# Kernel tuning notes

Measured on AMD Instinct MI355X. Metric: run time of the kernel, lower is better.

The kernel has to match this reference:

```python
import jax, jax.numpy as jnp
import numpy as np

N_ATOMS = 100000   # real atoms (index 0 is padding row -> total rows N_ATOMS+1)
N_BONDS = 200000   # real directed bonds (index 0 is padding row)
MAX_NB = 6
HIDDEN = 300
ATOM_FDIM = 133
BOND_FDIM = 147
DEPTH = 3
N_MOLS = 5000
ATOMS_PER_MOL = N_ATOMS // N_MOLS


def setup_inputs() -> dict:
    key = jax.random.key(0)
    ks = jax.random.split(key, 8)
    f_atoms = jax.random.normal(ks[0], (N_ATOMS + 1, ATOM_FDIM), dtype=jnp.float32)
    f_atoms = f_atoms.at[0].set(0.0)  # chemprop zero-padding row
    f_bonds = jax.random.normal(ks[1], (N_BONDS + 1, BOND_FDIM), dtype=jnp.float32)
    f_bonds = f_bonds.at[0].set(0.0)
    # weights (Linear stored as [in, out]); bias=False for W_i/W_h, W_o has bias
    W_i = jax.random.normal(ks[2], (BOND_FDIM, HIDDEN), dtype=jnp.float32) * 0.05
    W_h = jax.random.normal(ks[3], (HIDDEN, HIDDEN), dtype=jnp.float32) * 0.05
    W_o = jax.random.normal(ks[4], (ATOM_FDIM + HIDDEN, HIDDEN), dtype=jnp.float32) * 0.05
    b_o = jnp.zeros((HIDDEN,), dtype=jnp.float32)
    # a2b: incoming bond ids per atom, padded with 0 (padding row of message is 0)
    a2b = jax.random.randint(ks[5], (N_ATOMS + 1, MAX_NB), 0, N_BONDS + 1, dtype=jnp.int32)
    a2b = a2b.at[0].set(0)
    # b2a: source atom of each bond
    b2a = jax.random.randint(ks[6], (N_BONDS + 1,), 1, N_ATOMS + 1, dtype=jnp.int32)
    b2a = b2a.at[0].set(0)
    # b2revb: reverse-bond pairing; bonds (2k+1, 2k+2) are partners, 0 -> 0
    idx = jnp.arange(N_BONDS + 1, dtype=jnp.int32)
    b2revb = jnp.where(idx == 0, 0, ((idx - 1) ^ 1) + 1).astype(jnp.int32)
    # molecule segment id for each real atom (replaces a_scope loop)
    mol_ids = (jnp.arange(N_ATOMS, dtype=jnp.int32) // ATOMS_PER_MOL).astype(jnp.int32)
    return {"f_atoms": f_atoms, "f_bonds": f_bonds, "W_i": W_i, "W_h": W_h,
            "W_o": W_o, "b_o": b_o, "a2b": a2b, "b2a": b2a, "b2revb": b2revb,
            "mol_ids": mol_ids}


def reference(f_atoms, f_bonds, W_i, W_h, W_o, b_o, a2b, b2a, b2revb, mol_ids):
    # input = act(W_i(f_bonds))  (ReLU, bias=False)
    inp = jax.nn.relu(f_bonds @ W_i)                    # [B+1, H]
    message = inp
    for _ in range(DEPTH - 1):
        nei = message[a2b]                              # [A+1, MAX_NB, H] gather
        a_message = nei.sum(axis=1)                     # [A+1, H]
        message = a_message[b2a] - message[b2revb]      # [B+1, H]
        message = jax.nn.relu(inp + message @ W_h)      # skip-connection + act
    # final atom readout
    a_message = message[a2b].sum(axis=1)                # [A+1, H]
    a_input = jnp.concatenate([f_atoms, a_message], axis=1)
    atom_hiddens = jax.nn.relu(a_input @ W_o + b_o)     # [A+1, H]
    # per-molecule mean pooling over real atoms (rows 1:)
    real = atom_hiddens[1:]                             # [A, H]
    sums = jax.ops.segment_sum(real, mol_ids, num_segments=N_MOLS)
    counts = jax.ops.segment_sum(jnp.ones((N_ATOMS,), dtype=real.dtype), mol_ids,
                                 num_segments=N_MOLS)
    mol_vecs = sums / jnp.maximum(counts, 1.0)[:, None]  # [N_MOLS, H]
    return mol_vecs
```

## Files before the change

### kernel.cpp

```cpp
#include <hip/hip_runtime.h>
#include <hip/hip_bf16.h>

#define N_ATOMS   100000
#define N_BONDS   200000
#define MAX_NB    6
#define HIDDEN    300
#define ATOM_FDIM 133
#define BOND_FDIM 147
#define N_MOLS    5000
#define APM       20

#define MB_ROWS (N_BONDS + 1)
#define MA_ROWS (N_ATOMS + 1)

#define CHUNKS_B 1280
#define EPS      308
#define ROWP     65

typedef unsigned short bf16_t;
typedef __attribute__((ext_vector_type(8))) __bf16 bf16x8;
typedef __attribute__((ext_vector_type(4))) float  float4v;
typedef __attribute__((ext_vector_type(2))) unsigned int uint2v;

__device__ __forceinline__ float bf2f(unsigned short u) {
    union { unsigned int i; float f; } x; x.i = ((unsigned int)u) << 16; return x.f;
}
__device__ __forceinline__ unsigned short f2bf(float f) {
    union { float f; unsigned int i; } x; x.f = f;
    unsigned int r = x.i + 0x7FFFu + ((x.i >> 16) & 1u);
    return (unsigned short)(r >> 16);
}
__device__ __forceinline__ float lo_f(unsigned int u) {
    union { unsigned int i; float f; } x; x.i = u << 16; return x.f;
}
__device__ __forceinline__ float hi_f(unsigned int u) {
    union { unsigned int i; float f; } x; x.i = u & 0xffff0000u; return x.f;
}

__device__ __forceinline__ void gload8(uint2v& d, const void* a) {
    asm volatile("global_load_dwordx2 %0, %1, off"
                 : "=v"(d) : "v"(a) : "memory");
}
#define VM_DRAIN() do {                                      \
    asm volatile("s_waitcnt vmcnt(0)" ::: "memory");         \
    __builtin_amdgcn_sched_barrier(0);                       \
} while (0)

__global__ __launch_bounds__(256) void prep_w(
    const float* __restrict__ W, bf16_t* __restrict__ dst, int K,
    int total_chunks, int perm)
{
    int idx = blockIdx.x * 256 + threadIdx.x;
    if (idx >= total_chunks) return;
    int kb  = idx / CHUNKS_B;
    int c   = idx - kb * CHUNKS_B;
    int cq  = c / 320;
    int col = c - cq * 320;
    unsigned short v[8];
    #pragma unroll
    for (int j = 0; j < 8; ++j) {
        int k = kb * 32 + cq * 8 + j;
        int ksrc;
        if (perm) ksrc = (k < 133) ? k : ((k >= 136 && k < 436) ? k - 3 : -1);
        else      ksrc = (k < K) ? k : -1;
        float f = (ksrc >= 0 && col < HIDDEN) ? W[(size_t)ksrc * HIDDEN + col] : 0.f;
        v[j] = f2bf(f);
    }
    bf16_t* p = dst + (size_t)idx * 8;
    *(ushort4*)(p)     = make_ushort4(v[0], v[1], v[2], v[3]);
    *(ushort4*)(p + 4) = make_ushort4(v[4], v[5], v[6], v[7]);
}

template<int MODE, int KB>
__global__ __launch_bounds__(512, 4) void gemm_mfma(
    const float* __restrict__ Af,
    const bf16_t* __restrict__ Ab1, const bf16_t* __restrict__ Ab2,
    const int* __restrict__ b2a, const int* __restrict__ b2revb,
    const bf16_t* __restrict__ WB, const float* __restrict__ bias,
    const bf16_t* __restrict__ addend, bf16_t* __restrict__ Y,
    int M)
{
    const int S = HIDDEN;
    constexpr int QG    = KB * 4;
    constexpr int TASKS = 64 * QG;
    constexpr int NT    = (TASKS + 511) / 512;
    constexpr int T1  = 64 * 17;
    constexpr int T2  = 64 * 39;
    constexpr int NT1 = (T1 + 511) / 512;
    constexpr int NT2 = (T2 + 511) / 512;
    constexpr int ASZ   = QG * ROWP * 16;
    constexpr int LDS_BYTES = (ASZ > 16 * EPS * 4) ? ASZ : 16 * EPS * 4;
    __shared__ __align__(16) char lds_pool[LDS_BYTES];
    bf16_t* As  = (bf16_t*)lds_pool;
    float*  epi = (float*)lds_pool;
    __shared__ int rowmap[128];

    const int tid  = threadIdx.x;
    const int lane = tid & 63;
    const int w    = tid >> 6;
    const int wm   = w >> 2;
    const int wn   = w & 3;
    const int lrow = lane & 15;
    const int q    = lane >> 4;
    const int bm   = blockIdx.x * 64;

    if (MODE == 1) {
        if (tid < 64) {
            int sr = bm + tid;
            rowmap[tid] = (sr < M) ? b2a[sr] : 0;
        } else if (tid < 128) {
            int sr = bm + tid - 64;
            rowmap[tid] = (sr < M) ? b2revb[sr] : 0;
        }
        __syncthreads();
    }

    const bf16_t* wptr = WB + (size_t)(q * 320 + wn * 80 + lrow) * 8;
    bf16x8 bcur[5], bnxt[5];

    uint2v A0[MODE == 1 ? NT : 1], A1[MODE == 1 ? NT : 1];
    uint2v C0g[MODE == 1 ? NT : 1], C1g[MODE == 1 ? NT : 1];
    float  F[MODE == 0 ? NT : 1][8];
    float  Ff[MODE == 2 ? NT1 : 1][8];
    ushort4 U0[MODE == 2 ? NT2 : 1], U1[MODE == 2 ? NT2 : 1];
    const ushort4 zz = make_ushort4(0, 0, 0, 0);

    if (MODE == 1) {
        #pragma unroll
        for (int i = 0; i < NT; ++i) {
            int t = tid + i * 512;
            int row = t / QG, qg = t - row * QG, k0 = qg * 8;
            const bf16_t* pa = Ab1 + (size_t)rowmap[row]      * S;
            const bf16_t* pc = Ab2 + (size_t)rowmap[64 + row] * S;
            gload8(A0[i],  (k0 + 4 <= S) ? (const void*)(pa + k0)     : (const void*)Ab1);
            gload8(A1[i],  (k0 + 8 <= S) ? (const void*)(pa + k0 + 4) : (const void*)Ab1);
            gload8(C0g[i], (k0 + 4 <= S) ? (const void*)(pc + k0)     : (const void*)Ab1);
            gload8(C1g[i], (k0 + 8 <= S) ? (const void*)(pc + k0 + 4) : (const void*)Ab1);
        }
        VM_DRAIN();
    } else if (MODE == 0) {
        #pragma unroll
        for (int i = 0; i < NT; ++i) {
            int t = tid + i * 512;
            t = (t < TASKS) ? t : TASKS - 1;
            int row = t / QG, qg = t - row * QG, k0 = qg * 8;
            int srow = bm + row;
            int rbase = srow * BOND_FDIM;
            #pragma unroll
            for (int j = 0; j < 8; ++j) {
                int k = k0 + j;
                F[i][j] = Af[(srow < M && k < BOND_FDIM) ? rbase + k : 0];
            }
        }
    } else {
        #pragma unroll
        for (int i = 0; i < NT1; ++i) {
            int u = tid + i * 512;
            u = (u < T1) ? u : T1 - 1;
            int row = u / 17, qg = u - row * 17, k0 = qg * 8;
            int srow = bm + row;
            int rbase = srow * ATOM_FDIM;
            #pragma unroll
            for (int j = 0; j < 8; ++j) {
                int k = k0 + j;
                Ff[i][j] = Af[(srow < M && k < ATOM_FDIM) ? rbase + k : 0];
            }
        }
        #pragma unroll
        for (int i = 0; i < NT2; ++i) {
            int u = tid + i * 512;
            u = (u < T2) ? u : T2 - 1;
            int row = u / 39, off = (u - row * 39) * 8;
            int srow = bm + row;
            const bf16_t* pm = Ab1 + (size_t)srow * S;
            bool ok = (srow < M);
            U0[i] = *(const ushort4*)((ok && off + 4 <= S) ? pm + off     : Ab1);
            U1[i] = *(const ushort4*)((ok && off + 8 <= S) ? pm + off + 4 : Ab1);
        }
    }
    #pragma unroll
    for (int nt = 0; nt < 5; ++nt)
        bcur[nt] = *(const bf16x8*)(wptr + nt * 128);
    if (MODE != 1) __builtin_amdgcn_sched_barrier(0);

    if (MODE == 1) {
        #pragma unroll
        for (int i = 0; i < NT; ++i) {
            int t = tid + i * 512;
            int row = t / QG, qg = t - row * QG;
            unsigned short av[8];
            av[0] = f2bf(lo_f(A0[i].x) - lo_f(C0g[i].x));
            av[1] = f2bf(hi_f(A0[i].x) - hi_f(C0g[i].x));
            av[2] = f2bf(lo_f(A0[i].y) - lo_f(C0g[i].y));
            av[3] = f2bf(hi_f(A0[i].y) - hi_f(C0g[i].y));
            av[4] = f2bf(lo_f(A1[i].x) - lo_f(C1g[i].x));
            av[5] = f2bf(hi_f(A1[i].x) - hi_f(C1g[i].x));
            av[6] = f2bf(lo_f(A1[i].y) - lo_f(C1g[i].y));
            av[7] = f2bf(hi_f(A1[i].y) - hi_f(C1g[i].y));
            bf16_t* dst = As + (size_t)(qg * ROWP + row) * 8;
            *(ushort4*)(dst)     = make_ushort4(av[0], av[1], av[2], av[3]);
            *(ushort4*)(dst + 4) = make_ushort4(av[4], av[5], av[6], av[7]);
        }
    } else if (MODE == 0) {
        #pragma unroll
        for (int i = 0; i < NT; ++i) {
            int t = tid + i * 512;
            t = (t < TASKS) ? t : TASKS - 1;
            int row = t / QG, qg = t - row * QG;
            unsigned short av[8];
            #pragma unroll
            for (int j = 0; j < 8; ++j) av[j] = f2bf(F[i][j]);
            bf16_t* dst = As + (size_t)(qg * ROWP + row) * 8;
            *(ushort4*)(dst)     = make_ushort4(av[0], av[1], av[2], av[3]);
            *(ushort4*)(dst + 4) = make_ushort4(av[4], av[5], av[6], av[7]);
        }
    } else {
        #pragma unroll
        for (int i = 0; i < NT1; ++i) {
            int u = tid + i * 512;
            u = (u < T1) ? u : T1 - 1;
            int row = u / 17, qg = u - row * 17;
            unsigned short av[8];
            #pragma unroll
            for (int j = 0; j < 8; ++j) av[j] = f2bf(Ff[i][j]);
            bf16_t* dst = As + (size_t)(qg * ROWP + row) * 8;
            *(ushort4*)(dst)     = make_ushort4(av[0], av[1], av[2], av[3]);
            *(ushort4*)(dst + 4) = make_ushort4(av[4], av[5], av[6], av[7]);
        }
        #pragma unroll
        for (int i = 0; i < NT2; ++i) {
            int u = tid + i * 512;
            u = (u < T2) ? u : T2 - 1;
            int row = u / 39, qg = 17 + (u - row * 39);
            bf16_t* dst = As + (size_t)(qg * ROWP + row) * 8;
            *(ushort4*)(dst)     = U0[i];
            *(ushort4*)(dst + 4) = U1[i];
        }
    }

    float4v acc[2][5];
    #pragma unroll
    for (int i = 0; i < 2; ++i)
        #pragma unroll
        for (int j = 0; j < 5; ++j) {
            float4v z = {0.f, 0.f, 0.f, 0.f};
            acc[i][j] = z;
        }

    __syncthreads();

    #pragma unroll
    for (int kb = 0; kb < KB; ++kb) {
        const bf16_t* abase = As + (size_t)((kb * 4 + q) * ROWP + wm * 32 + lrow) * 8;
        bf16x8 af0 = *(const bf16x8*)(abase);
        bf16x8 af1 = *(const bf16x8*)(abase + 16 * 8);
        if (kb + 1 < KB) {
            const bf16_t* wnx = wptr + (size_t)(kb + 1) * (CHUNKS_B * 8);
            #pragma unroll
            for (int nt = 0; nt < 5; ++nt)
                bnxt[nt] = *(const bf16x8*)(wnx + nt * 128);
        }
        #pragma unroll
        for (int nt = 0; nt < 5; ++nt) {
            if (wn * 80 + nt * 16 < HIDDEN) {
                acc[0][nt] = __builtin_amdgcn_mfma_f32_16x16x32_bf16(af0, bcur[nt], acc[0][nt], 0, 0, 0);
                acc[1][nt] = __builtin_amdgcn_mfma_f32_16x16x32_bf16(af1, bcur[nt], acc[1][nt], 0, 0, 0);
            }
        }
        if (kb + 1 < KB) {
            #pragma unroll
            for (int nt = 0; nt < 5; ++nt) bcur[nt] = bnxt[nt];
        }
    }

    __syncthreads();
    #pragma unroll
    for (int mt = 0; mt < 2; ++mt) {
        for (int wh = 0; wh < 2; ++wh) {
            if (wm == wh) {
                #pragma unroll
                for (int nt = 0; nt < 5; ++nt) {
                    const int c0 = wn * 80 + nt * 16;
                    if (c0 < HIDDEN) {
                        #pragma unroll
                        for (int r = 0; r < 4; ++r)
                            epi[(q * 4 + r) * EPS + c0 + lrow] = acc[mt][nt][r];
                    }
                }
            }
            __syncthreads();
            const int row0 = bm + wh * 32 + mt * 16;
            for (int s = tid; s < 16 * 75; s += 512) {
                int rr = s / 75;
                int c4 = s - rr * 75;
                int grow = row0 + rr;
                if (grow < M) {
                    float4 v = *(const float4*)&epi[rr * EPS + c4 * 4];
                    if (MODE == 1) {
                        ushort4 ad = *(const ushort4*)(addend + (size_t)grow * S + c4 * 4);
                        v.x += bf2f(ad.x); v.y += bf2f(ad.y);
                        v.z += bf2f(ad.z); v.w += bf2f(ad.w);
                    }
                    if (MODE == 2) {
                        float4 bv = *(const float4*)(bias + c4 * 4);
                        v.x += bv.x; v.y += bv.y; v.z += bv.z; v.w += bv.w;
                    }
                    ushort4 o;
                    o.x = f2bf(v.x > 0.f ? v.x : 0.f);
                    o.y = f2bf(v.y > 0.f ? v.y : 0.f);
                    o.z = f2bf(v.z > 0.f ? v.z : 0.f);
                    o.w = f2bf(v.w > 0.f ? v.w : 0.f);
                    *(ushort4*)(Y + (size_t)grow * S + c4 * 4) = o;
                }
            }
            __syncthreads();
        }
    }
}

__global__ __launch_bounds__(256, 4) void aggregate_k(
    const bf16_t* __restrict__ msg, const int* __restrict__ a2b,
    bf16_t* __restrict__ amsg)
{
    constexpr int TOT  = MA_ROWS * 25;
    constexpr int HALF = (TOT + 1) / 2;
    int i0 = blockIdx.x * 256 + threadIdx.x;
    if (i0 >= HALF) return;
    int  i1   = i0 + HALF;
    bool has1 = (i1 < TOT);
    int  i1c  = has1 ? i1 : 0;
    int a0 = i0 / 25,  g0 = i0 - a0 * 25,  c0 = g0 * 12;
    int a1 = i1c / 25, g1 = i1c - a1 * 25, c1 = g1 * 12;

    const int* nb0 = a2b + (size_t)a0 * MAX_NB;
    const int* nb1 = a2b + (size_t)a1 * MAX_NB;
    int b0[MAX_NB], b1[MAX_NB];
    #pragma unroll
    for (int j = 0; j < MAX_NB; ++j) { b0[j] = nb0[j]; b1[j] = nb1[j]; }
    int chk = 0;
    #pragma unroll
    for (int j = 0; j < MAX_NB; ++j) chk |= b0[j] | b1[j];
    asm volatile("" :: "v"(chk));
    __builtin_amdgcn_sched_barrier(0);

    uint2v R0[MAX_NB][3], R1[MAX_NB][3];
    #pragma unroll
    for (int j = 0; j < MAX_NB; ++j) {
        const bf16_t* p = msg + (size_t)b0[j] * HIDDEN + c0;
        gload8(R0[j][0], p);
        gload8(R0[j][1], p + 4);
        gload8(R0[j][2], p + 8);
    }
    #pragma unroll
    for (int j = 0; j < MAX_NB; ++j) {
        const bf16_t* p = msg + (size_t)b1[j] * HIDDEN + c1;
        gload8(R1[j][0], p);
        gload8(R1[j][1], p + 4);
        gload8(R1[j][2], p + 8);
    }
    VM_DRAIN();

    float s0[12], s1[12];
    #pragma unroll
    for (int k = 0; k < 12; ++k) { s0[k] = 0.f; s1[k] = 0.f; }
    #pragma unroll
    for (int j = 0; j < MAX_NB; ++j) {
        #pragma unroll
        for (int h = 0; h < 3; ++h) {
            s0[h*4+0] += lo_f(R0[j][h].x); s0[h*4+1] += hi_f(R0[j][h].x);
            s0[h*4+2] += lo_f(R0[j][h].y); s0[h*4+3] += hi_f(R0[j][h].y);
            s1[h*4+0] += lo_f(R1[j][h].x); s1[h*4+1] += hi_f(R1[j][h].x);
            s1[h*4+2] += lo_f(R1[j][h].y); s1[h*4+3] += hi_f(R1[j][h].y);
        }
    }
    bf16_t* o0 = amsg + (size_t)a0 * HIDDEN + c0;
    *(ushort4*)(o0)     = make_ushort4(f2bf(s0[0]), f2bf(s0[1]), f2bf(s0[2]),  f2bf(s0[3]));
    *(ushort4*)(o0 + 4) = make_ushort4(f2bf(s0[4]), f2bf(s0[5]), f2bf(s0[6]),  f2bf(s0[7]));
    *(ushort4*)(o0 + 8) = make_ushort4(f2bf(s0[8]), f2bf(s0[9]), f2bf(s0[10]), f2bf(s0[11]));
    if (has1) {
        bf16_t* o1 = amsg + (size_t)a1 * HIDDEN + c1;
        *(ushort4*)(o1)     = make_ushort4(f2bf(s1[0]), f2bf(s1[1]), f2bf(s1[2]),  f2bf(s1[3]));
        *(ushort4*)(o1 + 4) = make_ushort4(f2bf(s1[4]), f2bf(s1[5]), f2bf(s1[6]),  f2bf(s1[7]));
        *(ushort4*)(o1 + 8) = make_ushort4(f2bf(s1[8]), f2bf(s1[9]), f2bf(s1[10]), f2bf(s1[11]));
    }
}

__global__ __launch_bounds__(256) void mol_mean_k(
    const bf16_t* __restrict__ atom_h, float* __restrict__ out)
{
    int idx = blockIdx.x * blockDim.x + threadIdx.x;
    if (idx >= N_MOLS * 75) return;
    int m  = idx / 75;
    int c4 = idx - m * 75;
    const bf16_t* base = atom_h + (size_t)(1 + m * APM) * HIDDEN + c4 * 4;
    float4 s = make_float4(0.f, 0.f, 0.f, 0.f);
    #pragma unroll
    for (int i = 0; i < APM; ++i) {
        ushort4 u = *(const ushort4*)(base + (size_t)i * HIDDEN);
        s.x += bf2f(u.x); s.y += bf2f(u.y); s.z += bf2f(u.z); s.w += bf2f(u.w);
    }
    const float inv = 1.0f / (float)APM;
    s.x *= inv; s.y *= inv; s.z *= inv; s.w *= inv;
    *(float4*)(out + (size_t)m * HIDDEN + c4 * 4) = s;
}

extern "C" void kernel_launch(void* const* d_in, const int* in_sizes, int n_in,
                              void* d_out, int out_size, void* d_ws, size_t ws_size,
                              hipStream_t stream)
{
    const float* f_atoms = (const float*)d_in[0];
    const float* f_bonds = (const float*)d_in[1];
    const float* W_i     = (const float*)d_in[2];
    const float* W_h     = (const float*)d_in[3];
    const float* W_o     = (const float*)d_in[4];
    const float* b_o     = (const float*)d_in[5];
    const int*   a2b     = (const int*)d_in[6];
    const int*   b2a     = (const int*)d_in[7];
    const int*   b2revb  = (const int*)d_in[8];
    float* out = (float*)d_out;

    char* base = (char*)d_ws;
    const size_t SZ_BOND_B = (((size_t)MB_ROWS * HIDDEN * sizeof(bf16_t)) + 255) & ~(size_t)255;
    bf16_t* inp  = (bf16_t*)(base);
    bf16_t* msgA = (bf16_t*)(base + SZ_BOND_B);
    bf16_t* amsg = (bf16_t*)(base + 2 * SZ_BOND_B);

    char* scratch = (char*)d_out;
    bf16_t* Wib = (bf16_t*)(scratch);
    bf16_t* Whb = (bf16_t*)(scratch + 102400);
    bf16_t* Wob = (bf16_t*)(scratch + 307200);

    dim3 blk512(512), blk256(256);
    const int gb = (MB_ROWS + 63) / 64;
    const int ga = (MA_ROWS + 63) / 64;
    const int agg_tasks  = ((MA_ROWS * 25) + 1) / 2;
    int agg_blocks  = (agg_tasks + 255) / 256;
    int mean_blocks = (N_MOLS * 75 + 255) / 256;

    prep_w<<<(5  * CHUNKS_B + 255) / 256, blk256, 0, stream>>>(W_i, Wib, BOND_FDIM, 5 * CHUNKS_B, 0);
    prep_w<<<(10 * CHUNKS_B + 255) / 256, blk256, 0, stream>>>(W_h, Whb, HIDDEN, 10 * CHUNKS_B, 0);
    prep_w<<<(14 * CHUNKS_B + 255) / 256, blk256, 0, stream>>>(W_o, Wob, 436, 14 * CHUNKS_B, 1);

    gemm_mfma<0, 5><<<gb, blk512, 0, stream>>>(
        f_bonds, nullptr, nullptr, nullptr, nullptr,
        Wib, nullptr, nullptr, inp, MB_ROWS);

    aggregate_k<<<agg_blocks, blk256, 0, stream>>>(inp, a2b, amsg);
    gemm_mfma<1, 10><<<gb, blk512, 0, stream>>>(
        nullptr, amsg, inp, b2a, b2revb,
        Whb, nullptr, inp, msgA, MB_ROWS);

    aggregate_k<<<agg_blocks, blk256, 0, stream>>>(msgA, a2b, amsg);
    gemm_mfma<1, 10><<<gb, blk512, 0, stream>>>(
        nullptr, amsg, msgA, b2a, b2revb,
        Whb, nullptr, inp, inp, MB_ROWS);

    aggregate_k<<<agg_blocks, blk256, 0, stream>>>(inp, a2b, amsg);
    gemm_mfma<2, 14><<<ga, blk512, 0, stream>>>(
        f_atoms, amsg, nullptr, nullptr, nullptr,
        Wob, b_o, nullptr, msgA, MA_ROWS);

    mol_mean_k<<<mean_blocks, blk256, 0, stream>>>(msgA, out);
}
```

Before: 811.7 us.

## Stage GEMM A-tile in two K halves to shrink LDS footprint

```diff
diff --git a/kernel.cpp b/kernel.cpp
--- a/kernel.cpp
+++ b/kernel.cpp
@@ -21,6 +21,8 @@
 typedef __attribute__((ext_vector_type(8))) __bf16 bf16x8;
 typedef __attribute__((ext_vector_type(4))) float  float4v;
 typedef __attribute__((ext_vector_type(2))) unsigned int uint2v;
+
+template<int N> struct IC { static constexpr int value = N; };
 
 __device__ __forceinline__ float bf2f(unsigned short u) {
     union { unsigned int i; float f; } x; x.i = ((unsigned int)u) << 16; return x.f;
@@ -71,7 +73,7 @@
     *(ushort4*)(p + 4) = make_ushort4(v[4], v[5], v[6], v[7]);
 }
 
-template<int MODE, int KB>
+template<int MODE, int KB, int KH1>
 __global__ __launch_bounds__(512, 4) void gemm_mfma(
     const float* __restrict__ Af,
     const bf16_t* __restrict__ Ab1, const bf16_t* __restrict__ Ab2,
@@ -81,14 +83,10 @@
     int M)
 {
     const int S = HIDDEN;
-    constexpr int QG    = KB * 4;
-    constexpr int TASKS = 64 * QG;
-    constexpr int NT    = (TASKS + 511) / 512;
-    constexpr int T1  = 64 * 17;
-    constexpr int T2  = 64 * 39;
-    constexpr int NT1 = (T1 + 511) / 512;
-    constexpr int NT2 = (T2 + 511) / 512;
-    constexpr int ASZ   = QG * ROWP * 16;
+    constexpr int KH2 = KB - KH1;
+    constexpr int QH1 = KH1 * 4, QH2 = KH2 * 4;
+    constexpr int QGM = (QH1 > QH2) ? QH1 : QH2;
+    constexpr int ASZ = QGM * ROWP * 16;
     constexpr int LDS_BYTES = (ASZ > 16 * EPS * 4) ? ASZ : 16 * EPS * 4;
     __shared__ __align__(16) char lds_pool[LDS_BYTES];
     bf16_t* As  = (bf16_t*)lds_pool;
@@ -116,127 +114,6 @@
     }
 
     const bf16_t* wptr = WB + (size_t)(q * 320 + wn * 80 + lrow) * 8;
-    bf16x8 bcur[5], bnxt[5];
-
-    uint2v A0[MODE == 1 ? NT : 1], A1[MODE == 1 ? NT : 1];
-    uint2v C0g[MODE == 1 ? NT : 1], C1g[MODE == 1 ? NT : 1];
-    float  F[MODE == 0 ? NT : 1][8];
-    float  Ff[MODE == 2 ? NT1 : 1][8];
-    ushort4 U0[MODE == 2 ? NT2 : 1], U1[MODE == 2 ? NT2 : 1];
-    const ushort4 zz = make_ushort4(0, 0, 0, 0);
-
-    if (MODE == 1) {
-        #pragma unroll
-        for (int i = 0; i < NT; ++i) {
-            int t = tid + i * 512;
-            int row = t / QG, qg = t - row * QG, k0 = qg * 8;
-            const bf16_t* pa = Ab1 + (size_t)rowmap[row]      * S;
-            const bf16_t* pc = Ab2 + (size_t)rowmap[64 + row] * S;
-            gload8(A0[i],  (k0 + 4 <= S) ? (const void*)(pa + k0)     : (const void*)Ab1);
-            gload8(A1[i],  (k0 + 8 <= S) ? (const void*)(pa + k0 + 4) : (const void*)Ab1);
-            gload8(C0g[i], (k0 + 4 <= S) ? (const void*)(pc + k0)     : (const void*)Ab1);
-            gload8(C1g[i], (k0 + 8 <= S) ? (const void*)(pc + k0 + 4) : (const void*)Ab1);
-        }
-        VM_DRAIN();
-    } else if (MODE == 0) {
-        #pragma unroll
-        for (int i = 0; i < NT; ++i) {
-            int t = tid + i * 512;
-            t = (t < TASKS) ? t : TASKS - 1;
-            int row = t / QG, qg = t - row * QG, k0 = qg * 8;
-            int srow = bm + row;
-            int rbase = srow * BOND_FDIM;
-            #pragma unroll
-            for (int j = 0; j < 8; ++j) {
-                int k = k0 + j;
-                F[i][j] = Af[(srow < M && k < BOND_FDIM) ? rbase + k : 0];
-            }
-        }
-    } else {
-        #pragma unroll
-        for (int i = 0; i < NT1; ++i) {
-            int u = tid + i * 512;
-            u = (u < T1) ? u : T1 - 1;
-            int row = u / 17, qg = u - row * 17, k0 = qg * 8;
-            int srow = bm + row;
-            int rbase = srow * ATOM_FDIM;
-            #pragma unroll
-            for (int j = 0; j < 8; ++j) {
-                int k = k0 + j;
-                Ff[i][j] = Af[(srow < M && k < ATOM_FDIM) ? rbase + k : 0];
-            }
-        }
-        #pragma unroll
-        for (int i = 0; i < NT2; ++i) {
-            int u = tid + i * 512;
-            u = (u < T2) ? u : T2 - 1;
-            int row = u / 39, off = (u - row * 39) * 8;
-            int srow = bm + row;
-            const bf16_t* pm = Ab1 + (size_t)srow * S;
-            bool ok = (srow < M);
-            U0[i] = *(const ushort4*)((ok && off + 4 <= S) ? pm + off     : Ab1);
-            U1[i] = *(const ushort4*)((ok && off + 8 <= S) ? pm + off + 4 : Ab1);
-        }
-    }
-    #pragma unroll
-    for (int nt = 0; nt < 5; ++nt)
-        bcur[nt] = *(const bf16x8*)(wptr + nt * 128);
-    if (MODE != 1) __builtin_amdgcn_sched_barrier(0);
-
-    if (MODE == 1) {
-        #pragma unroll
-        for (int i = 0; i < NT; ++i) {
-            int t = tid + i * 512;
-            int row = t / QG, qg = t - row * QG;
-            unsigned short av[8];
-            av[0] = f2bf(lo_f(A0[i].x) - lo_f(C0g[i].x));
-            av[1] = f2bf(hi_f(A0[i].x) - hi_f(C0g[i].x));
-            av[2] = f2bf(lo_f(A0[i].y) - lo_f(C0g[i].y));
-            av[3] = f2bf(hi_f(A0[i].y) - hi_f(C0g[i].y));
-            av[4] = f2bf(lo_f(A1[i].x) - lo_f(C1g[i].x));
-            av[5] = f2bf(hi_f(A1[i].x) - hi_f(C1g[i].x));
-            av[6] = f2bf(lo_f(A1[i].y) - lo_f(C1g[i].y));
-            av[7] = f2bf(hi_f(A1[i].y) - hi_f(C1g[i].y));
-            bf16_t* dst = As + (size_t)(qg * ROWP + row) * 8;
-            *(ushort4*)(dst)     = make_ushort4(av[0], av[1], av[2], av[3]);
-            *(ushort4*)(dst + 4) = make_ushort4(av[4], av[5], av[6], av[7]);
-        }
-    } else if (MODE == 0) {
-        #pragma unroll
-        for (int i = 0; i < NT; ++i) {
-            int t = tid + i * 512;
-            t = (t < TASKS) ? t : TASKS - 1;
-            int row = t / QG, qg = t - row * QG;
-            unsigned short av[8];
-            #pragma unroll
-            for (int j = 0; j < 8; ++j) av[j] = f2bf(F[i][j]);
-            bf16_t* dst = As + (size_t)(qg * ROWP + row) * 8;
-            *(ushort4*)(dst)     = make_ushort4(av[0], av[1], av[2], av[3]);
-            *(ushort4*)(dst + 4) = make_ushort4(av[4], av[5], av[6], av[7]);
-        }
-    } else {
-        #pragma unroll
-        for (int i = 0; i < NT1; ++i) {
-            int u = tid + i * 512;
-            u = (u < T1) ? u : T1 - 1;
-            int row = u / 17, qg = u - row * 17;
-            unsigned short av[8];
-            #pragma unroll
-            for (int j = 0; j < 8; ++j) av[j] = f2bf(Ff[i][j]);
-            bf16_t* dst = As + (size_t)(qg * ROWP + row) * 8;
-            *(ushort4*)(dst)     = make_ushort4(av[0], av[1], av[2], av[3]);
-            *(ushort4*)(dst + 4) = make_ushort4(av[4], av[5], av[6], av[7]);
-        }
-        #pragma unroll
-        for (int i = 0; i < NT2; ++i) {
-            int u = tid + i * 512;
-            u = (u < T2) ? u : T2 - 1;
-            int row = u / 39, qg = 17 + (u - row * 39);
-            bf16_t* dst = As + (size_t)(qg * ROWP + row) * 8;
-            *(ushort4*)(dst)     = U0[i];
-            *(ushort4*)(dst + 4) = U1[i];
-        }
-    }
 
     float4v acc[2][5];
     #pragma unroll
@@ -247,30 +124,187 @@
             acc[i][j] = z;
         }
 
+    auto stage_half = [&](auto QG0c, auto QGHc) {
+        constexpr int QG0 = decltype(QG0c)::value;
+        constexpr int QGH = decltype(QGHc)::value;
+        constexpr int TASKS = 64 * QGH;
+        constexpr int NT = (TASKS + 511) / 512;
+        #define ACT(tt) ((TASKS % 512 == 0) || ((tt) < TASKS))
+
+        if constexpr (MODE == 1) {
+            uint2v A0[NT], A1[NT], C0[NT], C1[NT];
+            #pragma unroll
+            for (int i = 0; i < NT; ++i) {
+                int t = tid + i * 512;
+                if (ACT(t)) {
+                    int row = t / QGH, ql = t - row * QGH;
+                    int k0 = (QG0 + ql) * 8;
+                    const bf16_t* pa = Ab1 + (size_t)rowmap[row]      * S;
+                    const bf16_t* pc = Ab2 + (size_t)rowmap[64 + row] * S;
+                    gload8(A0[i], (k0 + 4 <= S) ? (const void*)(pa + k0)     : (const void*)Ab1);
+                    gload8(A1[i], (k0 + 8 <= S) ? (const void*)(pa + k0 + 4) : (const void*)Ab1);
+                    gload8(C0[i], (k0 + 4 <= S) ? (const void*)(pc + k0)     : (const void*)Ab1);
+                    gload8(C1[i], (k0 + 8 <= S) ? (const void*)(pc + k0 + 4) : (const void*)Ab1);
+                }
+            }
+            VM_DRAIN();
+            #pragma unroll
+            for (int i = 0; i < NT; ++i) {
+                int t = tid + i * 512;
+                if (ACT(t)) {
+                    int row = t / QGH, ql = t - row * QGH;
+                    unsigned short av[8];
+                    av[0] = f2bf(lo_f(A0[i].x) - lo_f(C0[i].x));
+                    av[1] = f2bf(hi_f(A0[i].x) - hi_f(C0[i].x));
+                    av[2] = f2bf(lo_f(A0[i].y) - lo_f(C0[i].y));
+                    av[3] = f2bf(hi_f(A0[i].y) - hi_f(C0[i].y));
+                    av[4] = f2bf(lo_f(A1[i].x) - lo_f(C1[i].x));
+                    av[5] = f2bf(hi_f(A1[i].x) - hi_f(C1[i].x));
+                    av[6] = f2bf(lo_f(A1[i].y) - lo_f(C1[i].y));
+                    av[7] = f2bf(hi_f(A1[i].y) - hi_f(C1[i].y));
+                    bf16_t* dst = As + (size_t)(ql * ROWP + row) * 8;
+                    *(ushort4*)(dst)     = make_ushort4(av[0], av[1], av[2], av[3]);
+                    *(ushort4*)(dst + 4) = make_ushort4(av[4], av[5], av[6], av[7]);
+                }
+            }
+        } else if constexpr (MODE == 0) {
+            float F[NT][8];
+            #pragma unroll
+            for (int i = 0; i < NT; ++i) {
+                int t = tid + i * 512;
+                if (ACT(t)) {
+                    int row = t / QGH, ql = t - row * QGH, k0 = (QG0 + ql) * 8;
+                    int srow = bm + row;
+                    int rbase = srow * BOND_FDIM;
+                    #pragma unroll
+                    for (int j = 0; j < 8; ++j) {
+                        int k = k0 + j;
+                        F[i][j] = Af[(srow < M && k < BOND_FDIM) ? rbase + k : 0];
+                    }
+                }
+            }
+            #pragma unroll
+            for (int i = 0; i < NT; ++i) {
+                int t = tid + i * 512;
+                if (ACT(t)) {
+                    int row = t / QGH, ql = t - row * QGH;
+                    unsigned short av[8];
+                    #pragma unroll
+                    for (int j = 0; j < 8; ++j) av[j] = f2bf(F[i][j]);
+                    bf16_t* dst = As + (size_t)(ql * ROWP + row) * 8;
+                    *(ushort4*)(dst)     = make_ushort4(av[0], av[1], av[2], av[3]);
+                    *(ushort4*)(dst + 4) = make_ushort4(av[4], av[5], av[6], av[7]);
+                }
+            }
+        } else {
+            constexpr int NF = (QG0 >= 17) ? 0 : ((17 - QG0 < QGH) ? 17 - QG0 : QGH);
+            constexpr int TB = QGH - NF;
+            if constexpr (NF > 0) {
+                constexpr int T1 = 64 * NF;
+                constexpr int NT1 = (T1 + 511) / 512;
+                float Ff[NT1][8];
+                #pragma unroll
+                for (int i = 0; i < NT1; ++i) {
+                    int u = tid + i * 512;
+                    if ((T1 % 512 == 0) || u < T1) {
+                        int row = u / NF, f = u - row * NF, k0 = (QG0 + f) * 8;
+                        int srow = bm + row;
+                        int rbase = srow * ATOM_FDIM;
+                        #pragma unroll
+                        for (int j = 0; j < 8; ++j) {
+                            int k = k0 + j;
+                            Ff[i][j] = Af[(srow < M && k < ATOM_FDIM) ? rbase + k : 0];
+                        }
+                    }
+                }
+                #pragma unroll
+                for (int i = 0; i < NT1; ++i) {
+                    int u = tid + i * 512;
+                    if ((T1 % 512 == 0) || u < T1) {
+                        int row = u / NF, f = u - row * NF;
+                        unsigned short av[8];
+                        #pragma unroll
+                        for (int j = 0; j < 8; ++j) av[j] = f2bf(Ff[i][j]);
+                        bf16_t* dst = As + (size_t)(f * ROWP + row) * 8;
+                        *(ushort4*)(dst)     = make_ushort4(av[0], av[1], av[2], av[3]);
+                        *(ushort4*)(dst + 4) = make_ushort4(av[4], av[5], av[6], av[7]);
+                    }
+                }
+            }
+            if constexpr (TB > 0) {
+                constexpr int T2 = 64 * TB;
+                constexpr int NT2 = (T2 + 511) / 512;
+                ushort4 U0[NT2], U1[NT2];
+                #pragma unroll
+                for (int i = 0; i < NT2; ++i) {
+                    int u = tid + i * 512;
+                    if ((T2 % 512 == 0) || u < T2) {
+                        int row = u / TB, b = u - row * TB;
+                        int off = (QG0 + NF + b) * 8 - 136;
+                        int srow = bm + row;
+                        const bf16_t* pm = Ab1 + (size_t)srow * S;
+                        bool ok = (srow < M);
+                        U0[i] = *(const ushort4*)((ok && off + 4 <= S) ? pm + off     : Ab1);
+                        U1[i] = *(const ushort4*)((ok && off + 8 <= S) ? pm + off + 4 : Ab1);
+                    }
+                }
+                #pragma unroll
+                for (int i = 0; i < NT2; ++i) {
+                    int u = tid + i * 512;
+                    if ((T2 % 512 == 0) || u < T2) {
+                        int row = u / TB, b = u - row * TB;
+                        int ql = NF + b;
+                        bf16_t* dst = As + (size_t)(ql * ROWP + row) * 8;
+                        *(ushort4*)(dst)     = U0[i];
+                        *(ushort4*)(dst + 4) = U1[i];
+                    }
+                }
+            }
+        }
+        #undef ACT
+    };
+
+    auto run_kloop = [&](auto KB0c, auto KB1c) {
+        constexpr int KB0 = decltype(KB0c)::value;
+        constexpr int KB1 = decltype(KB1c)::value;
+        bf16x8 bcur[5], bnxt[5];
+        const bf16_t* w0 = wptr + (size_t)KB0 * (CHUNKS_B * 8);
+        #pragma unroll
+        for (int nt = 0; nt < 5; ++nt)
+            bcur[nt] = *(const bf16x8*)(w0 + nt * 128);
+        #pragma unroll
+        for (int kb = KB0; kb < KB1; ++kb) {
+            const bf16_t* abase = As + (size_t)(((kb - KB0) * 4 + q) * ROWP + wm * 32 + lrow) * 8;
+            bf16x8 af0 = *(const bf16x8*)(abase);
+            bf16x8 af1 = *(const bf16x8*)(abase + 16 * 8);
+            if (kb + 1 < KB1) {
+                const bf16_t* wnx = wptr + (size_t)(kb + 1) * (CHUNKS_B * 8);
+                #pragma unroll
+                for (int nt = 0; nt < 5; ++nt)
+                    bnxt[nt] = *(const bf16x8*)(wnx + nt * 128);
+            }
+            #pragma unroll
+            for (int nt = 0; nt < 5; ++nt) {
+                if (wn * 80 + nt * 16 < HIDDEN) {
+                    acc[0][nt] = __builtin_amdgcn_mfma_f32_16x16x32_bf16(af0, bcur[nt], acc[0][nt], 0, 0, 0);
+                    acc[1][nt] = __builtin_amdgcn_mfma_f32_16x16x32_bf16(af1, bcur[nt], acc[1][nt], 0, 0, 0);
+                }
+            }
+            if (kb + 1 < KB1) {
+                #pragma unroll
+                for (int nt = 0; nt < 5; ++nt) bcur[nt] = bnxt[nt];
+            }
+        }
+    };
+
+    stage_half(IC<0>{}, IC<QH1>{});
     __syncthreads();
-
-    #pragma unroll
-    for (int kb = 0; kb < KB; ++kb) {
-        const bf16_t* abase = As + (size_t)((kb * 4 + q) * ROWP + wm * 32 + lrow) * 8;
-        bf16x8 af0 = *(const bf16x8*)(abase);
-        bf16x8 af1 = *(const bf16x8*)(abase + 16 * 8);
-        if (kb + 1 < KB) {
-            const bf16_t* wnx = wptr + (size_t)(kb + 1) * (CHUNKS_B * 8);
-            #pragma unroll
-            for (int nt = 0; nt < 5; ++nt)
-                bnxt[nt] = *(const bf16x8*)(wnx + nt * 128);
-        }
-        #pragma unroll
-        for (int nt = 0; nt < 5; ++nt) {
-            if (wn * 80 + nt * 16 < HIDDEN) {
-                acc[0][nt] = __builtin_amdgcn_mfma_f32_16x16x32_bf16(af0, bcur[nt], acc[0][nt], 0, 0, 0);
-                acc[1][nt] = __builtin_amdgcn_mfma_f32_16x16x32_bf16(af1, bcur[nt], acc[1][nt], 0, 0, 0);
-            }
-        }
-        if (kb + 1 < KB) {
-            #pragma unroll
-            for (int nt = 0; nt < 5; ++nt) bcur[nt] = bnxt[nt];
-        }
+    run_kloop(IC<0>{}, IC<KH1>{});
+    if constexpr (KH2 > 0) {
+        __syncthreads();
+        stage_half(IC<QH1>{}, IC<QH2>{});
+        __syncthreads();
+        run_kloop(IC<KH1>{}, IC<KB>{});
     }
 
     __syncthreads();
@@ -441,22 +475,22 @@
     prep_w<<<(10 * CHUNKS_B + 255) / 256, blk256, 0, stream>>>(W_h, Whb, HIDDEN, 10 * CHUNKS_B, 0);
     prep_w<<<(14 * CHUNKS_B + 255) / 256, blk256, 0, stream>>>(W_o, Wob, 436, 14 * CHUNKS_B, 1);
 
-    gemm_mfma<0, 5><<<gb, blk512, 0, stream>>>(
+    gemm_mfma<0, 5, 5><<<gb, blk512, 0, stream>>>(
         f_bonds, nullptr, nullptr, nullptr, nullptr,
         Wib, nullptr, nullptr, inp, MB_ROWS);
 
     aggregate_k<<<agg_blocks, blk256, 0, stream>>>(inp, a2b, amsg);
-    gemm_mfma<1, 10><<<gb, blk512, 0, stream>>>(
+    gemm_mfma<1, 10, 5><<<gb, blk512, 0, stream>>>(
         nullptr, amsg, inp, b2a, b2revb,
         Whb, nullptr, inp, msgA, MB_ROWS);
 
     aggregate_k<<<agg_blocks, blk256, 0, stream>>>(msgA, a2b, amsg);
-    gemm_mfma<1, 10><<<gb, blk512, 0, stream>>>(
+    gemm_mfma<1, 10, 5><<<gb, blk512, 0, stream>>>(
         nullptr, amsg, msgA, b2a, b2revb,
         Whb, nullptr, inp, inp, MB_ROWS);
 
     aggregate_k<<<agg_blocks, blk256, 0, stream>>>(inp, a2b, amsg);
-    gemm_mfma<2, 14><<<ga, blk512, 0, stream>>>(
+    gemm_mfma<2, 14, 7><<<ga, blk512, 0, stream>>>(
         f_atoms, amsg, nullptr, nullptr, nullptr,
         Wob, b_o, nullptr, msgA, MA_ROWS);
 
```

Result: no change. 824.1 us (+1.5%).
